# Kernel tuning notes

Measured on AMD Instinct MI355X. Metric: run time of the kernel, lower is better.

The kernel has to match this reference:

```python
import jax, jax.numpy as jnp
import numpy as np

B, L, D, Z, V, N, MAXPOS = 8, 2048, 1024, 128, 2048, 16, 2048


def setup_inputs():
    key = jax.random.key(0)
    ks = jax.random.split(key, 16)
    std = 0.02
    return {
        "x": jax.random.normal(ks[0], (B, L, D), jnp.float32),
        "norm1_w": jnp.ones((D,), jnp.float32),
        "norm1_b": jnp.zeros((D,), jnp.float32),
        "ema_delta": jax.random.normal(ks[1], (D, N), jnp.float32) * 0.2,
        "ema_alpha": jax.random.normal(ks[2], (D, N), jnp.float32) * 0.2,
        "ema_beta": jax.random.normal(ks[3], (D, N), jnp.float32) * 0.02,
        "ema_gamma": jax.random.normal(ks[4], (D, N), jnp.float32),
        "ema_omega": jax.random.normal(ks[5], (D,), jnp.float32),
        "vproj_w": jax.random.normal(ks[6], (D, V), jnp.float32) * std,
        "vproj_b": jnp.zeros((V,), jnp.float32),
        "mx_w": jax.random.normal(ks[7], (D, Z + V + 2 * D), jnp.float32) * std,
        "mx_b": jnp.zeros((Z + V + 2 * D,), jnp.float32),
        "h_w": jax.random.normal(ks[8], (V, D), jnp.float32) * std,
        "h_b": jnp.zeros((D,), jnp.float32),
        "att_gamma": jax.random.normal(ks[9], (2, Z), jnp.float32) * std,
        "att_beta": jnp.zeros((2, Z), jnp.float32),
        "rel_bias": jax.random.normal(ks[10], (2 * MAXPOS - 1,), jnp.float32) * std,
        "norm2_w": jnp.ones((D,), jnp.float32),
        "norm2_b": jnp.zeros((D,), jnp.float32),
        "ff_w1": jax.random.normal(ks[11], (D, 2 * D), jnp.float32) * std,
        "ff_b1": jnp.zeros((2 * D,), jnp.float32),
        "ff_w2": jax.random.normal(ks[12], (2 * D, D), jnp.float32) * std,
        "ff_b2": jnp.zeros((D,), jnp.float32),
    }


def _layernorm(x, w, b):
    mu = jnp.mean(x, -1, keepdims=True)
    var = jnp.mean((x - mu) ** 2, -1, keepdims=True)
    return (x - mu) * jax.lax.rsqrt(var + 1e-5) * w + b


def reference(x, norm1_w, norm1_b, ema_delta, ema_alpha, ema_beta, ema_gamma, ema_omega,
              vproj_w, vproj_b, mx_w, mx_b, h_w, h_b, att_gamma, att_beta, rel_bias,
              norm2_w, norm2_b, ff_w1, ff_b1, ff_w2, ff_b2):
    residual = x
    xn = _layernorm(x, norm1_w, norm1_b)                       # prenorm
    v = jax.nn.silu(xn @ vproj_w + vproj_b)                    # (B L V)

    # --- MultiHeadEMA (damped EMA state space) via FFT convolution ---
    p = jax.nn.sigmoid(ema_delta)                              # (D N)
    q = 1.0 - p * jax.nn.sigmoid(ema_alpha)                    # (D N) in (0,1)
    t = jnp.arange(L, dtype=jnp.float32)
    vander = jnp.exp(t[None, None, :] * jnp.log(q)[:, :, None])       # (D N L)
    kern = jnp.einsum('dnl,dn->dl', (p * ema_beta)[:, :, None] * vander,
                      ema_gamma * np.float32(1.0 / np.sqrt(N)))        # (D L)
    xT = jnp.swapaxes(xn, 1, 2)                                # (B D L)
    k_f = jnp.fft.rfft(kern, n=2 * L)
    x_f = jnp.fft.rfft(xT, n=2 * L)
    ema = jnp.fft.irfft(x_f * k_f, n=2 * L)[..., :L]           # causal conv
    mx = jax.nn.silu(jnp.swapaxes(ema, 1, 2) + xn * ema_omega) # (B L D)

    # --- moving-average gated attention ---
    base = mx @ mx_w + mx_b                                    # (B L D+Z+V+D)
    u, zr, hx = jnp.split(base, [D, D + Z + V], axis=-1)
    u = jax.nn.sigmoid(u)                                      # update gate
    zr = jax.nn.silu(zr)
    z, r = zr[..., :Z], zr[..., Z:]                            # (B L Z), (B L V)
    zqk = z[:, :, None, :] * att_gamma + att_beta              # (B L 2 Z)
    qh, kh = zqk[:, :, 0, :], zqk[:, :, 1, :]

    # simple relative positional bias: Toeplitz bias[i,j] = b[L-1 + j - i]
    bseg = rel_bias[MAXPOS - L:MAXPOS + L - 1]                 # (2L-1,)
    idx = (L - 1) + jnp.arange(L)[None, :] - jnp.arange(L)[:, None]
    bias = bseg[idx]                                           # (L L)

    qk = jnp.einsum('blz,bmz->blm', qh * np.float32(Z ** -0.5), kh) + bias
    attn = jax.nn.softmax(qk, axis=-1)                         # (B L L)
    h = jnp.einsum('blm,bmv->blv', attn, v)                    # (B L V)
    h = jax.nn.silu(hx + (h * r) @ h_w + h_b)                  # (B L D)
    out = residual + u * (h - residual)                        # addcmul gate

    # --- prenorm FFN residual block (expand=2, silu) ---
    y = _layernorm(out, norm2_w, norm2_b)
    y = jax.nn.silu(y @ ff_w1 + ff_b1) @ ff_w2 + ff_b2
    return out + y
```

## Files before the change

kernel.cpp:

```cpp
#include <hip/hip_runtime.h>
#include <hip/hip_bf16.h>
#include <cstdint>

#define B_ 8
#define L_ 2048
#define D_ 1024
#define Z_ 128
#define V_ 2048
#define N_ 16
#define NC_ 16
#define CL_ 128

typedef unsigned short ushort_t;
typedef __attribute__((ext_vector_type(8))) short short8;
typedef __attribute__((ext_vector_type(4))) float floatx4;

__device__ __forceinline__ float b2f(ushort_t u){ union{float f;unsigned i;}x; x.i=((unsigned)u)<<16; return x.f; }
__device__ __forceinline__ ushort_t f2b(float f){ union{float f;unsigned i;}x; x.f=f; unsigned r=(x.i+0x7fffu+((x.i>>16)&1u))>>16; return (ushort_t)r; }
__device__ __forceinline__ float sigmoidf_(float x){ return 1.0f/(1.0f+__expf(-x)); }
__device__ __forceinline__ float siluf_(float x){ return x/(1.0f+__expf(-x)); }

#define GLL16(g,l) __builtin_amdgcn_global_load_lds( \
    (const __attribute__((address_space(1))) void*)(g), \
    (__attribute__((address_space(3))) void*)(l), 16, 0, 0)

__device__ __forceinline__ float blockSum(float v){
  #pragma unroll
  for(int off=32;off;off>>=1) v += __shfl_xor(v,off);
  __shared__ float sm[4];
  __syncthreads();
  if((threadIdx.x&63)==0) sm[threadIdx.x>>6]=v;
  __syncthreads();
  return (sm[0]+sm[1])+(sm[2]+sm[3]);
}
__device__ __forceinline__ float blockMax(float v){
  #pragma unroll
  for(int off=32;off;off>>=1) v = fmaxf(v,__shfl_xor(v,off));
  __shared__ float sm[4];
  __syncthreads();
  if((threadIdx.x&63)==0) sm[threadIdx.x>>6]=v;
  __syncthreads();
  return fmaxf(fmaxf(sm[0],sm[1]),fmaxf(sm[2],sm[3]));
}

__global__ __launch_bounds__(256) void ln_kernel(const float* __restrict__ in,
    const float* __restrict__ w, const float* __restrict__ b,
    ushort_t* __restrict__ o16){
  const int row = blockIdx.x;
  const int t = threadIdx.x;
  const float* p = in + (size_t)row*D_;
  float4 v = *reinterpret_cast<const float4*>(p + t*4);
  float s = (v.x+v.y)+(v.z+v.w);
  s = blockSum(s);
  float mu = s*(1.0f/D_);
  float dx=v.x-mu, dy=v.y-mu, dz=v.z-mu, dw=v.w-mu;
  float ss = dx*dx+dy*dy+dz*dz+dw*dw;
  ss = blockSum(ss);
  float inv = rsqrtf(ss*(1.0f/D_)+1e-5f);
  float4 wv = *reinterpret_cast<const float4*>(w + t*4);
  float4 bv = *reinterpret_cast<const float4*>(b + t*4);
  union{ushort_t u[4]; uint2 q;} o;
  o.u[0]=f2b(dx*inv*wv.x+bv.x); o.u[1]=f2b(dy*inv*wv.y+bv.y);
  o.u[2]=f2b(dz*inv*wv.z+bv.z); o.u[3]=f2b(dw*inv*wv.w+bv.w);
  *reinterpret_cast<uint2*>(o16+(size_t)row*D_+t*4)=o.q;
}

__global__ __launch_bounds__(256) void transpose_w(const float* __restrict__ in,
    ushort_t* __restrict__ out, int R, int C){
  __shared__ float tile[32][33];
  int bx=blockIdx.x*32, by=blockIdx.y*32;
  int tx=threadIdx.x&31, ty=threadIdx.x>>5;
  #pragma unroll
  for(int i=0;i<32;i+=8) tile[ty+i][tx] = in[(size_t)(by+ty+i)*C + bx+tx];
  __syncthreads();
  #pragma unroll
  for(int i=0;i<32;i+=8) out[(size_t)(bx+ty+i)*R + by+tx] = f2b(tile[tx][ty+i]);
}

__global__ __launch_bounds__(256) void ema_setup(const float* __restrict__ delta,
    const float* __restrict__ alpha, const float* __restrict__ beta,
    const float* __restrict__ gamma, float* __restrict__ qarr,
    float* __restrict__ warr, float* __restrict__ qC){
  int i = blockIdx.x*256+threadIdx.x;
  if(i>=D_*N_) return;
  float p = sigmoidf_(delta[i]);
  float q = 1.0f - p*sigmoidf_(alpha[i]);
  qarr[i]=q; warr[i]=p*beta[i]*gamma[i]*0.25f;
  qC[i]=powf(q,(float)CL_);
}

__global__ __launch_bounds__(256) void ema_pass1(const ushort_t* __restrict__ xn,
    const float* __restrict__ qarr, float* __restrict__ E){
  int idx = blockIdx.x*256+threadIdx.x;
  int d = idx & (D_-1); int c = (idx>>10)&15; int b = idx>>14;
  const ushort_t* xp = xn + ((size_t)b*L_ + c*CL_)*D_ + d;
  float q[N_], s[N_];
  #pragma unroll
  for(int n=0;n<N_;n++){ q[n]=qarr[d*N_+n]; s[n]=0.0f; }
  for(int i=0;i<CL_;i+=8){
    float xv[8];
    #pragma unroll
    for(int j=0;j<8;j++) xv[j]=b2f(xp[(size_t)(i+j)*D_]);
    #pragma unroll
    for(int j=0;j<8;j++){
      #pragma unroll
      for(int n=0;n<N_;n++) s[n]=fmaf(q[n],s[n],xv[j]);
    }
  }
  float* Ep = E + (((size_t)b*NC_+c)*N_)*D_ + d;
  #pragma unroll
  for(int n=0;n<N_;n++) Ep[(size_t)n*D_]=s[n];
}

__global__ __launch_bounds__(256) void ema_pass2(const float* __restrict__ E,
    const float* __restrict__ qC, float* __restrict__ In){
  int idx = blockIdx.x*256+threadIdx.x;
  int d = idx & (D_-1); int b = idx>>10;
  float S[N_], qc[N_];
  #pragma unroll
  for(int n=0;n<N_;n++){ S[n]=0.0f; qc[n]=qC[d*N_+n]; }
  for(int c=0;c<NC_;c++){
    size_t base = (((size_t)b*NC_+c)*N_)*D_ + d;
    #pragma unroll
    for(int n=0;n<N_;n++) In[base+(size_t)n*D_]=S[n];
    #pragma unroll
    for(int n=0;n<N_;n++) S[n]=fmaf(qc[n],S[n],E[base+(size_t)n*D_]);
  }
}

__global__ __launch_bounds__(256) void ema_pass3_mx(const ushort_t* __restrict__ xn,
    const float* __restrict__ qarr, const float* __restrict__ warr,
    const float* __restrict__ In, const float* __restrict__ omega,
    ushort_t* __restrict__ mx){
  int idx = blockIdx.x*256+threadIdx.x;
  int d = idx & (D_-1); int c = (idx>>10)&15; int b = idx>>14;
  const ushort_t* xp = xn + ((size_t)b*L_ + c*CL_)*D_ + d;
  ushort_t* op = mx + ((size_t)b*L_ + c*CL_)*D_ + d;
  size_t base = (((size_t)b*NC_+c)*N_)*D_ + d;
  float om = omega[d];
  float q[N_], w[N_], s[N_];
  #pragma unroll
  for(int n=0;n<N_;n++){ q[n]=qarr[d*N_+n]; w[n]=warr[d*N_+n]; s[n]=In[base+(size_t)n*D_]; }
  for(int i=0;i<CL_;i+=8){
    float xv[8];
    #pragma unroll
    for(int j=0;j<8;j++) xv[j]=b2f(xp[(size_t)(i+j)*D_]);
    #pragma unroll
    for(int j=0;j<8;j++){
      float a=0.0f;
      #pragma unroll
      for(int n=0;n<N_;n++){ s[n]=fmaf(q[n],s[n],xv[j]); a=fmaf(w[n],s[n],a); }
      op[(size_t)(i+j)*D_]=f2b(siluf_(a + xv[j]*om));
    }
  }
}

__global__ __launch_bounds__(256) void softmax_kernel(const float* __restrict__ qk,
    ushort_t* __restrict__ attn){
  size_t row = blockIdx.x;
  const float* p = qk + row*(size_t)L_;
  int t = threadIdx.x;
  float vals[8];
  #pragma unroll
  for(int i=0;i<8;i++) vals[i]=p[i*256+t];
  float m=-__builtin_inff();
  #pragma unroll
  for(int i=0;i<8;i++) m=fmaxf(m,vals[i]);
  m = blockMax(m);
  float s=0.0f;
  #pragma unroll
  for(int i=0;i<8;i++){ vals[i]=__expf(vals[i]-m); s+=vals[i]; }
  s = blockSum(s);
  float inv = 1.0f/s;
  ushort_t* q = attn + row*(size_t)L_;
  #pragma unroll
  for(int i=0;i<8;i++) q[i*256+t]=f2b(vals[i]*inv);
}

#define SBAR() do{ __builtin_amdgcn_sched_barrier(0); \
    asm volatile("" ::: "memory"); \
    __builtin_amdgcn_s_barrier(); \
    asm volatile("" ::: "memory"); \
    __builtin_amdgcn_sched_barrier(0); }while(0)
#define VMW(n) asm volatile("s_waitcnt vmcnt(" #n ")" ::: "memory")

#define BAR_ACQ(vm) do{ \
    asm volatile("s_waitcnt vmcnt(" #vm ")" ::: "memory"); \
    __builtin_amdgcn_s_barrier(); \
    __builtin_amdgcn_sched_barrier(0); }while(0)
#define BAR_REL() do{ \
    __builtin_amdgcn_sched_barrier(0); \
    asm volatile("" ::: "memory"); \
    __builtin_amdgcn_s_barrier(); \
    asm volatile("" ::: "memory"); }while(0)

template<class Epi>
__global__ __launch_bounds__(256) void gemm_nt(const ushort_t* __restrict__ A,
    const ushort_t* __restrict__ B, int M, int N, int K, Epi epi){
  __shared__ __align__(16) ushort_t As[2][128*64];
  __shared__ __align__(16) ushort_t Bs[2][128*64];
  const int t = threadIdx.x;
  const int wave=t>>6, lane=t&63, quad=lane>>4, l16=lane&15;
  const int bm=blockIdx.x*128, bn=blockIdx.y*128;
  const int wm=(wave>>1)*64, wn=(wave&1)*64;
  const int srow = wave*32 + (lane>>3);
  const int schk = ((lane&7) ^ (lane>>3)) * 8;
  const ushort_t* gA[4]; const ushort_t* gB[4];
  ushort_t *lA[4], *lB[4];
  #pragma unroll
  for(int i=0;i<4;i++){
    gA[i] = A + (size_t)(bm+srow+i*8)*K + schk;
    gB[i] = B + (size_t)(bn+srow+i*8)*K + schk;
    lA[i] = &As[0][(wave*32+i*8)*64];
    lB[i] = &Bs[0][(wave*32+i*8)*64];
  }
  const ushort_t* ra[2][4]; const ushort_t* rb[2][4];
  #pragma unroll
  for(int h=0;h<2;h++)
    #pragma unroll
    for(int i=0;i<4;i++){
      int rrA = wm+i*16+l16, rrB = wn+i*16+l16;
      ra[h][i] = &As[0][rrA*64 + (((h*4+quad)^(rrA&7))*8)];
      rb[h][i] = &Bs[0][rrB*64 + (((h*4+quad)^(rrB&7))*8)];
    }
  floatx4 acc[4][4];
  #pragma unroll
  for(int i=0;i<4;i++)
    #pragma unroll
    for(int j=0;j<4;j++) acc[i][j]=(floatx4){0.f,0.f,0.f,0.f};

  const int nk = K>>6;
  #pragma unroll
  for(int i=0;i<4;i++){ GLL16(gA[i], lA[i]); GLL16(gB[i], lB[i]); }

  for(int t0=0;t0<nk;t0+=2){
    {
      const int k0=(t0+1)<<6;
      #pragma unroll
      for(int i=0;i<4;i++){ GLL16(gA[i]+k0, lA[i]+(128*64)); GLL16(gB[i]+k0, lB[i]+(128*64)); }
    }
    BAR_ACQ(8);
    #pragma unroll
    for(int h=0;h<2;h++){
      short8 af[4], bf[4];
      #pragma unroll
      for(int mt=0;mt<4;mt++) af[mt]=*reinterpret_cast<const short8*>(ra[h][mt]);
      #pragma unroll
      for(int nt=0;nt<4;nt++) bf[nt]=*reinterpret_cast<const short8*>(rb[h][nt]);
      #pragma unroll
      for(int mt=0;mt<4;mt++)
        #pragma unroll
        for(int nt=0;nt<4;nt++)
          acc[mt][nt]=__builtin_amdgcn_mfma_f32_16x16x32_bf16(af[mt],bf[nt],acc[mt][nt],0,0,0);
    }
    BAR_REL();
    if(t0+2<nk){
      const int k0=(t0+2)<<6;
      #pragma unroll
      for(int i=0;i<4;i++){ GLL16(gA[i]+k0, lA[i]); GLL16(gB[i]+k0, lB[i]); }
      BAR_ACQ(8);
    } else {
      BAR_ACQ(0);
    }
    #pragma unroll
    for(int h=0;h<2;h++){
      short8 af[4], bf[4];
      #pragma unroll
      for(int mt=0;mt<4;mt++) af[mt]=*reinterpret_cast<const short8*>(ra[h][mt]+(128*64));
      #pragma unroll
      for(int nt=0;nt<4;nt++) bf[nt]=*reinterpret_cast<const short8*>(rb[h][nt]+(128*64));
      #pragma unroll
      for(int mt=0;mt<4;mt++)
        #pragma unroll
        for(int nt=0;nt<4;nt++)
          acc[mt][nt]=__builtin_amdgcn_mfma_f32_16x16x32_bf16(af[mt],bf[nt],acc[mt][nt],0,0,0);
    }
    BAR_REL();
  }

  #pragma unroll
  for(int mt=0;mt<4;mt++)
    #pragma unroll
    for(int nt=0;nt<4;nt++)
      #pragma unroll
      for(int r=0;r<4;r++){
        int row=bm+wm+mt*16+quad*4+r;
        int col=bn+wn+nt*16+l16;
        epi(acc[mt][nt][r], row, col, 0);
      }
}


#define RDA(buf,kh,mh) \
  af[0]=pA##kh[(buf)*2048+((mh)*4+0)*128]; \
  af[1]=pA##kh[(buf)*2048+((mh)*4+1)*128]; \
  af[2]=pA##kh[(buf)*2048+((mh)*4+2)*128]; \
  af[3]=pA##kh[(buf)*2048+((mh)*4+3)*128];
#define RDB(buf,kh) \
  bf[0]=pB##kh[(buf)*2048+0*128]; \
  bf[1]=pB##kh[(buf)*2048+1*128]; \
  bf[2]=pB##kh[(buf)*2048+2*128]; \
  bf[3]=pB##kh[(buf)*2048+3*128];
#define MMA16(mh) \
  __builtin_amdgcn_s_setprio(1); \
  acc[(mh)*4+0][0]=__builtin_amdgcn_mfma_f32_16x16x32_bf16(af[0],bf[0],acc[(mh)*4+0][0],0,0,0); \
  acc[(mh)*4+0][1]=__builtin_amdgcn_mfma_f32_16x16x32_bf16(af[0],bf[1],acc[(mh)*4+0][1],0,0,0); \
  acc[(mh)*4+0][2]=__builtin_amdgcn_mfma_f32_16x16x32_bf16(af[0],bf[2],acc[(mh)*4+0][2],0,0,0); \
  acc[(mh)*4+0][3]=__builtin_amdgcn_mfma_f32_16x16x32_bf16(af[0],bf[3],acc[(mh)*4+0][3],0,0,0); \
  acc[(mh)*4+1][0]=__builtin_amdgcn_mfma_f32_16x16x32_bf16(af[1],bf[0],acc[(mh)*4+1][0],0,0,0); \
  acc[(mh)*4+1][1]=__builtin_amdgcn_mfma_f32_16x16x32_bf16(af[1],bf[1],acc[(mh)*4+1][1],0,0,0); \
  acc[(mh)*4+1][2]=__builtin_amdgcn_mfma_f32_16x16x32_bf16(af[1],bf[2],acc[(mh)*4+1][2],0,0,0); \
  acc[(mh)*4+1][3]=__builtin_amdgcn_mfma_f32_16x16x32_bf16(af[1],bf[3],acc[(mh)*4+1][3],0,0,0); \
  acc[(mh)*4+2][0]=__builtin_amdgcn_mfma_f32_16x16x32_bf16(af[2],bf[0],acc[(mh)*4+2][0],0,0,0); \
  acc[(mh)*4+2][1]=__builtin_amdgcn_mfma_f32_16x16x32_bf16(af[2],bf[1],acc[(mh)*4+2][1],0,0,0); \
  acc[(mh)*4+2][2]=__builtin_amdgcn_mfma_f32_16x16x32_bf16(af[2],bf[2],acc[(mh)*4+2][2],0,0,0); \
  acc[(mh)*4+2][3]=__builtin_amdgcn_mfma_f32_16x16x32_bf16(af[2],bf[3],acc[(mh)*4+2][3],0,0,0); \
  acc[(mh)*4+3][0]=__builtin_amdgcn_mfma_f32_16x16x32_bf16(af[3],bf[0],acc[(mh)*4+3][0],0,0,0); \
  acc[(mh)*4+3][1]=__builtin_amdgcn_mfma_f32_16x16x32_bf16(af[3],bf[1],acc[(mh)*4+3][1],0,0,0); \
  acc[(mh)*4+3][2]=__builtin_amdgcn_mfma_f32_16x16x32_bf16(af[3],bf[2],acc[(mh)*4+3][2],0,0,0); \
  acc[(mh)*4+3][3]=__builtin_amdgcn_mfma_f32_16x16x32_bf16(af[3],bf[3],acc[(mh)*4+3][3],0,0,0); \
  __builtin_amdgcn_s_setprio(0);
#define STG8(buf,k0) \
  GLL16(gA[0]+(k0), lA[0]+(buf)*16384); GLL16(gA[1]+(k0), lA[1]+(buf)*16384); \
  GLL16(gA[2]+(k0), lA[2]+(buf)*16384); GLL16(gA[3]+(k0), lA[3]+(buf)*16384); \
  GLL16(gB[0]+(k0), lB[0]+(buf)*16384); GLL16(gB[1]+(k0), lB[1]+(buf)*16384); \
  GLL16(gB[2]+(k0), lB[2]+(buf)*16384); GLL16(gB[3]+(k0), lB[3]+(buf)*16384);

#define TILE_S(buf,k0n) { \
  short8 af[4], bf[4]; \
  RDA(buf,0,0) RDB(buf,0) \
  STG8((buf)^1, k0n) \
  SBAR(); MMA16(0) SBAR(); \
  RDA(buf,0,1) \
  SBAR(); MMA16(1) SBAR(); \
  RDA(buf,1,0) RDB(buf,1) \
  SBAR(); MMA16(0) SBAR(); \
  RDA(buf,1,1) \
  SBAR(); MMA16(1) VMW(0); SBAR(); \
}
#define TILE_L(buf) { \
  short8 af[4], bf[4]; \
  RDA(buf,0,0) RDB(buf,0) \
  SBAR(); MMA16(0) SBAR(); \
  RDA(buf,0,1) \
  SBAR(); MMA16(1) SBAR(); \
  RDA(buf,1,0) RDB(buf,1) \
  SBAR(); MMA16(0) SBAR(); \
  RDA(buf,1,1) \
  SBAR(); MMA16(1) \
}

template<class Epi>
__global__ __launch_bounds__(512) void gemm_nt2(const ushort_t* __restrict__ A0,
    const ushort_t* __restrict__ B0, int M, int N, int K,
    size_t za, size_t zb, Epi epi){
  __shared__ __align__(16) ushort_t As[2*256*64];
  __shared__ __align__(16) ushort_t Bs[2*256*64];
  const int t = threadIdx.x;
  const int wave=t>>6, lane=t&63, quad=lane>>4, l16=lane&15;
  int bx, by;
  {
    int gx=gridDim.x, gy=gridDim.y;
    int f = blockIdx.y*gx + blockIdx.x;
    if((gy==4 || gy==8) && (gx%(32/gy))==0){
      int GW = 32/gy, nst = gx/GW;
      int s, r;
      if((nst&7)==0){ int xc=f&7; int j=f>>3; s = xc*(nst>>3) + (j>>5); r = j&31; }
      else { s = f>>5; r = f&31; }
      bx = s*GW + (r%GW); by = r/GW;
    } else { bx = blockIdx.x; by = blockIdx.y; }
  }
  const int z = blockIdx.z;
  const ushort_t* A = A0 + (size_t)z*za;
  const ushort_t* B = B0 + (size_t)z*zb;
  const int bm=bx*256, bn=by*256;
  const int wm=(wave>>2)*128, wn=(wave&3)*64;
  const int roff = lane>>3;
  const int goff = ((lane&7)^(lane>>3))*8;
  const ushort_t* gA[4]; const ushort_t* gB[4];
  ushort_t* lA[4]; ushort_t* lB[4];
  #pragma unroll
  for(int i=0;i<4;i++){
    gA[i] = A + (size_t)(bm + wave*32 + i*8 + roff)*K + goff;
    gB[i] = B + (size_t)(bn + wave*32 + i*8 + roff)*K + goff;
    lA[i] = As + (wave*32 + i*8)*64;
    lB[i] = Bs + (wave*32 + i*8)*64;
  }
  const short8* pA0 = reinterpret_cast<const short8*>(As) + (wm+l16)*8 + ((quad  )^(l16&7));
  const short8* pA1 = reinterpret_cast<const short8*>(As) + (wm+l16)*8 + ((quad^4)^(l16&7));
  const short8* pB0 = reinterpret_cast<const short8*>(Bs) + (wn+l16)*8 + ((quad  )^(l16&7));
  const short8* pB1 = reinterpret_cast<const short8*>(Bs) + (wn+l16)*8 + ((quad^4)^(l16&7));
  floatx4 acc[8][4];
  #pragma unroll
  for(int i=0;i<8;i++)
    #pragma unroll
    for(int j=0;j<4;j++) acc[i][j]=(floatx4){0.f,0.f,0.f,0.f};

  const int nkt = K>>6;
  STG8(0, 0)
  VMW(0); SBAR();

  for(int t0=0; t0+2<nkt; t0+=2){
    TILE_S(0,(t0+1)<<6)
    TILE_S(1,(t0+2)<<6)
  }
  TILE_S(0,(nkt-1)<<6)
  TILE_L(1)

  #pragma unroll
  for(int mt=0;mt<8;mt++)
    #pragma unroll
    for(int nt=0;nt<4;nt++)
      #pragma unroll
      for(int r=0;r<4;r++){
        int row=bm+wm+mt*16+quad*4+r;
        int col=bn+wn+nt*16+l16;
        epi(acc[mt][nt][r], row, col, z);
      }
}

struct EpiV {
  ushort_t* vT; const float* vb;
  __device__ void operator()(float v,int row,int col,int) const {
    float s = siluf_(v + vb[col]);
    int b = row>>11, l = row&(L_-1);
    vT[((size_t)b*V_ + col)*L_ + l] = f2b(s);
  }
};
struct EpiU {
  ushort_t* u; const float* mxb;
  __device__ void operator()(float v,int row,int col,int) const {
    u[(size_t)row*D_+col]=f2b(sigmoidf_(v+mxb[col]));
  }
};
struct EpiQKh {
  ushort_t* qh; ushort_t* kh; const float* mxb; const float* ag; const float* ab;
  __device__ void operator()(float v,int row,int col,int) const {
    float z=siluf_(v+mxb[col]);
    qh[(size_t)row*Z_+col]=f2b(z*ag[col]+ab[col]);
    kh[(size_t)row*Z_+col]=f2b(z*ag[Z_+col]+ab[Z_+col]);
  }
};
struct EpiR {
  ushort_t* r; const float* mxb;
  __device__ void operator()(float v,int row,int col,int) const {
    r[(size_t)row*V_+col]=f2b(siluf_(v+mxb[col]));
  }
};
struct EpiHx {
  ushort_t* hx; const float* mxb;
  __device__ void operator()(float v,int row,int col,int) const {
    hx[(size_t)row*D_+col]=f2b(v+mxb[col]);
  }
};
struct EpiQK {
  float* qk; const float* rb;
  __device__ void operator()(float v,int row,int col,int) const {
    qk[(size_t)row*L_+col] = v*0.08838834764831845f + rb[L_-1+col-row];
  }
};
struct EpiH {
  ushort_t* hr; const ushort_t* r;
  __device__ void operator()(float v,int row,int col,int z) const {
    size_t idx = ((size_t)z*L_ + row)*V_ + col;
    hr[idx] = f2b(v * b2f(r[idx]));
  }
};
struct EpiOut {
  float* out; const float* x; const ushort_t* u; const ushort_t* hx; const float* hb;
  __device__ void operator()(float v,int row,int col,int) const {
    size_t idx=(size_t)row*D_+col;
    float h2 = siluf_(b2f(hx[idx]) + v + hb[col]);
    float xv = x[idx];
    out[idx] = xv + b2f(u[idx])*(h2-xv);
  }
};
struct EpiF1 {
  ushort_t* f1; const float* b1;
  __device__ void operator()(float v,int row,int col,int) const {
    f1[(size_t)row*(2*D_)+col]=f2b(siluf_(v+b1[col]));
  }
};
struct EpiFinal {
  float* dout; const float* b2;
  __device__ void operator()(float v,int row,int col,int) const {
    size_t idx=(size_t)row*D_+col;
    dout[idx] = dout[idx] + v + b2[col];
  }
};

extern "C" void kernel_launch(void* const* d_in, const int* in_sizes, int n_in,
                              void* d_out, int out_size, void* d_ws, size_t ws_size,
                              hipStream_t stream){
  const float* x        = (const float*)d_in[0];
  const float* norm1_w  = (const float*)d_in[1];
  const float* norm1_b  = (const float*)d_in[2];
  const float* ema_delta= (const float*)d_in[3];
  const float* ema_alpha= (const float*)d_in[4];
  const float* ema_beta = (const float*)d_in[5];
  const float* ema_gamma= (const float*)d_in[6];
  const float* ema_omega= (const float*)d_in[7];
  const float* vproj_w  = (const float*)d_in[8];
  const float* vproj_b  = (const float*)d_in[9];
  const float* mx_w     = (const float*)d_in[10];
  const float* mx_b     = (const float*)d_in[11];
  const float* h_w      = (const float*)d_in[12];
  const float* h_b      = (const float*)d_in[13];
  const float* att_gamma= (const float*)d_in[14];
  const float* att_beta = (const float*)d_in[15];
  const float* rel_bias = (const float*)d_in[16];
  const float* norm2_w  = (const float*)d_in[17];
  const float* norm2_b  = (const float*)d_in[18];
  const float* ff_w1    = (const float*)d_in[19];
  const float* ff_b1    = (const float*)d_in[20];
  const float* ff_w2    = (const float*)d_in[21];
  const float* ff_b2    = (const float*)d_in[22];
  float* dout = (float*)d_out;
  char* ws = (char*)d_ws;

  size_t cur = 0;
  auto take = [&](size_t b)->size_t{ size_t o=cur; cur += (b+255)&~255ull; return o; };
  const size_t o_wvT  = take((size_t)V_*D_*2);
  const size_t o_wmxT = take((size_t)4224*D_*2);
  const size_t o_whT  = take((size_t)D_*V_*2);
  const size_t o_wf1T = take((size_t)2*D_*D_*2);
  const size_t o_wf2T = take((size_t)D_*2*D_*2);
  const size_t o_qarr = take((size_t)D_*N_*4);
  const size_t o_warr = take((size_t)D_*N_*4);
  const size_t o_qC   = take((size_t)D_*N_*4);
  const size_t globals_end = cur;

  int g = 0;
  size_t o_xn=0,o_mx=0,o_u=0,o_hx=0,o_r=0,o_qh=0,o_kh=0,o_qk=0,o_at=0;
  for(int cand=8; cand>=1; cand>>=1){
    cur = globals_end;
    size_t xn_o = take((size_t)cand*L_*D_*2);
    size_t mx_o = take((size_t)cand*L_*D_*2);
    size_t u_o  = take((size_t)cand*L_*D_*2);
    size_t hx_o = take((size_t)cand*L_*D_*2);
    size_t r_o  = take((size_t)cand*L_*V_*2);
    size_t qh_o = take((size_t)cand*L_*Z_*2);
    size_t kh_o = take((size_t)cand*L_*Z_*2);
    size_t qk_o, at_o;
    if(cand>=4){ qk_o = xn_o; at_o = xn_o + (size_t)L_*L_*4; }
    else { qk_o = take((size_t)L_*L_*4); at_o = take((size_t)L_*L_*2); }
    if(cur <= ws_size){
      g=cand; o_xn=xn_o; o_mx=mx_o; o_u=u_o; o_hx=hx_o; o_r=r_o;
      o_qh=qh_o; o_kh=kh_o; o_qk=qk_o; o_at=at_o; break;
    }
  }
  if(!g) return;

  ushort_t* wvT  = (ushort_t*)(ws+o_wvT);
  ushort_t* wmxT = (ushort_t*)(ws+o_wmxT);
  ushort_t* whT  = (ushort_t*)(ws+o_whT);
  ushort_t* wf1T = (ushort_t*)(ws+o_wf1T);
  ushort_t* wf2T = (ushort_t*)(ws+o_wf2T);
  float* qarr = (float*)(ws+o_qarr);
  float* warr = (float*)(ws+o_warr);
  float* qC   = (float*)(ws+o_qC);
  ushort_t* xn  = (ushort_t*)(ws+o_xn);
  ushort_t* mx  = (ushort_t*)(ws+o_mx);
  ushort_t* u16 = (ushort_t*)(ws+o_u);
  ushort_t* hx16= (ushort_t*)(ws+o_hx);
  ushort_t* r16 = (ushort_t*)(ws+o_r);
  ushort_t* qh  = (ushort_t*)(ws+o_qh);
  ushort_t* kh  = (ushort_t*)(ws+o_kh);
  float*    qk  = (float*)   (ws+o_qk);
  ushort_t* attn= (ushort_t*)(ws+o_at);
  float*    E   = (float*)(ws+o_u);
  float*    In  = (float*)(ws+o_hx);
  ushort_t* ybf = xn;
  ushort_t* f1  = r16;

  int nbat; ushort_t* attnB;
  if(g>=4){ nbat = g/2; attnB = mx; }
  else    { nbat = 1;   attnB = attn; }

  transpose_w<<<dim3(V_/32, D_/32), 256, 0, stream>>>(vproj_w, wvT, D_, V_);
  transpose_w<<<dim3(4224/32, D_/32), 256, 0, stream>>>(mx_w, wmxT, D_, 4224);
  transpose_w<<<dim3(D_/32, V_/32), 256, 0, stream>>>(h_w, whT, V_, D_);
  transpose_w<<<dim3((2*D_)/32, D_/32), 256, 0, stream>>>(ff_w1, wf1T, D_, 2*D_);
  transpose_w<<<dim3(D_/32, (2*D_)/32), 256, 0, stream>>>(ff_w2, wf2T, 2*D_, D_);
  ema_setup<<<(D_*N_)/256, 256, 0, stream>>>(ema_delta, ema_alpha, ema_beta, ema_gamma, qarr, warr, qC);

  for(int gi=0; gi<B_/g; ++gi){
    const int RG = g*L_;
    const float* x_g  = x    + (size_t)gi*RG*D_;
    float*       do_g = dout + (size_t)gi*RG*D_;
    ushort_t*    vT   = (ushort_t*)do_g;

    ln_kernel<<<RG, 256, 0, stream>>>(x_g, norm1_w, norm1_b, xn);
    ema_pass1<<<(g*NC_*D_)/256, 256, 0, stream>>>(xn, qarr, E);
    ema_pass2<<<(g*D_)/256, 256, 0, stream>>>(E, qC, In);
    ema_pass3_mx<<<(g*NC_*D_)/256, 256, 0, stream>>>(xn, qarr, warr, In, ema_omega, mx);

    { EpiV e{vT, vproj_b};
      gemm_nt2<<<dim3(RG/256, V_/256), 512, 0, stream>>>(xn, wvT, RG, V_, D_, 0, 0, e); }

    { EpiU e{u16, mx_b};
      gemm_nt2<<<dim3(RG/256, D_/256), 512, 0, stream>>>(mx, wmxT, RG, D_, D_, 0, 0, e); }
    { EpiQKh e{qh, kh, mx_b+D_, att_gamma, att_beta};
      gemm_nt<<<dim3(RG/128, Z_/128), 256, 0, stream>>>(mx, wmxT+(size_t)D_*D_, RG, Z_, D_, e); }
    { EpiR e{r16, mx_b+D_+Z_};
      gemm_nt2<<<dim3(RG/256, V_/256), 512, 0, stream>>>(mx, wmxT+(size_t)(D_+Z_)*D_, RG, V_, D_, 0, 0, e); }
    { EpiHx e{hx16, mx_b+D_+Z_+V_};
      gemm_nt2<<<dim3(RG/256, D_/256), 512, 0, stream>>>(mx, wmxT+(size_t)(D_+Z_+V_)*D_, RG, D_, D_, 0, 0, e); }

    for(int q0=0; q0<g; q0+=nbat){
      for(int bi=q0; bi<q0+nbat; ++bi){
        { EpiQK e{qk, rel_bias};
          gemm_nt<<<dim3(L_/128, L_/128), 256, 0, stream>>>(
            qh+(size_t)bi*L_*Z_, kh+(size_t)bi*L_*Z_, L_, L_, Z_, e); }
        softmax_kernel<<<L_, 256, 0, stream>>>(qk, attnB+(size_t)(bi-q0)*L_*L_);
      }
      { EpiH e{r16+(size_t)q0*L_*V_, r16+(size_t)q0*L_*V_};
        gemm_nt2<<<dim3(L_/256, V_/256, nbat), 512, 0, stream>>>(
          attnB, vT+(size_t)q0*V_*L_, L_, V_, L_,
          (size_t)L_*L_, (size_t)V_*L_, e); }
    }

    { EpiOut e{do_g, x_g, u16, hx16, h_b};
      gemm_nt2<<<dim3(RG/256, D_/256), 512, 0, stream>>>(r16, whT, RG, D_, V_, 0, 0, e); }
    ln_kernel<<<RG, 256, 0, stream>>>(do_g, norm2_w, norm2_b, ybf);
    { EpiF1 e{f1, ff_b1};
      gemm_nt2<<<dim3(RG/256, (2*D_)/256), 512, 0, stream>>>(ybf, wf1T, RG, 2*D_, D_, 0, 0, e); }
    { EpiFinal e{do_g, ff_b2};
      gemm_nt2<<<dim3(RG/256, D_/256), 512, 0, stream>>>(f1, wf2T, RG, D_, 2*D_, 0, 0, e); }
  }
}
```

Before: 1.354 ms.

## Split GEMM LDS tiles into k-halves and stagger async loads across phases

Reorganizes the 256x256 bf16 GEMM's shared-memory staging into two 32-wide k-halves, each with its own swizzle. Global-to-LDS loads for the next tile are now spread across the four MMA phases, with partial vmcnt waits instead of one full wait per tile. This aims to overlap memory traffic with MFMA work and shorten stalls at tile boundaries. It also drops the sched_barrier fences around the barriers, which gives the compiler more scheduling freedom but risks reordering LDS accesses across synchronisation points.

```diff
diff --git a/kernel.cpp b/kernel.cpp
--- a/kernel.cpp
+++ b/kernel.cpp
@@ -177,19 +177,13 @@
   for(int i=0;i<8;i++) q[i*256+t]=f2b(vals[i]*inv);
 }
 
-#define SBAR() do{ __builtin_amdgcn_sched_barrier(0); \
-    asm volatile("" ::: "memory"); \
-    __builtin_amdgcn_s_barrier(); \
-    asm volatile("" ::: "memory"); \
-    __builtin_amdgcn_sched_barrier(0); }while(0)
+#define BAR() __builtin_amdgcn_s_barrier()
 #define VMW(n) asm volatile("s_waitcnt vmcnt(" #n ")" ::: "memory")
 
 #define BAR_ACQ(vm) do{ \
     asm volatile("s_waitcnt vmcnt(" #vm ")" ::: "memory"); \
-    __builtin_amdgcn_s_barrier(); \
-    __builtin_amdgcn_sched_barrier(0); }while(0)
+    __builtin_amdgcn_s_barrier(); }while(0)
 #define BAR_REL() do{ \
-    __builtin_amdgcn_sched_barrier(0); \
     asm volatile("" ::: "memory"); \
     __builtin_amdgcn_s_barrier(); \
     asm volatile("" ::: "memory"); }while(0)
@@ -291,16 +285,16 @@
 }
 
 
-#define RDA(buf,kh,mh) \
-  af[0]=pA##kh[(buf)*2048+((mh)*4+0)*128]; \
-  af[1]=pA##kh[(buf)*2048+((mh)*4+1)*128]; \
-  af[2]=pA##kh[(buf)*2048+((mh)*4+2)*128]; \
-  af[3]=pA##kh[(buf)*2048+((mh)*4+3)*128];
-#define RDB(buf,kh) \
-  bf[0]=pB##kh[(buf)*2048+0*128]; \
-  bf[1]=pB##kh[(buf)*2048+1*128]; \
-  bf[2]=pB##kh[(buf)*2048+2*128]; \
-  bf[3]=pB##kh[(buf)*2048+3*128];
+#define RA4(buf,kh,mh) \
+  af[0]=pA8[(buf)*2048+(kh)*1024+((mh)*4+0)*64+rowA]; \
+  af[1]=pA8[(buf)*2048+(kh)*1024+((mh)*4+1)*64+rowA]; \
+  af[2]=pA8[(buf)*2048+(kh)*1024+((mh)*4+2)*64+rowA]; \
+  af[3]=pA8[(buf)*2048+(kh)*1024+((mh)*4+3)*64+rowA];
+#define RB4(buf,kh) \
+  bf[0]=pB8[(buf)*2048+(kh)*1024+0*64+rowB]; \
+  bf[1]=pB8[(buf)*2048+(kh)*1024+1*64+rowB]; \
+  bf[2]=pB8[(buf)*2048+(kh)*1024+2*64+rowB]; \
+  bf[3]=pB8[(buf)*2048+(kh)*1024+3*64+rowB];
 #define MMA16(mh) \
   __builtin_amdgcn_s_setprio(1); \
   acc[(mh)*4+0][0]=__builtin_amdgcn_mfma_f32_16x16x32_bf16(af[0],bf[0],acc[(mh)*4+0][0],0,0,0); \
@@ -320,42 +314,46 @@
   acc[(mh)*4+3][2]=__builtin_amdgcn_mfma_f32_16x16x32_bf16(af[3],bf[2],acc[(mh)*4+3][2],0,0,0); \
   acc[(mh)*4+3][3]=__builtin_amdgcn_mfma_f32_16x16x32_bf16(af[3],bf[3],acc[(mh)*4+3][3],0,0,0); \
   __builtin_amdgcn_s_setprio(0);
-#define STG8(buf,k0) \
-  GLL16(gA[0]+(k0), lA[0]+(buf)*16384); GLL16(gA[1]+(k0), lA[1]+(buf)*16384); \
-  GLL16(gA[2]+(k0), lA[2]+(buf)*16384); GLL16(gA[3]+(k0), lA[3]+(buf)*16384); \
-  GLL16(gB[0]+(k0), lB[0]+(buf)*16384); GLL16(gB[1]+(k0), lB[1]+(buf)*16384); \
-  GLL16(gB[2]+(k0), lB[2]+(buf)*16384); GLL16(gB[3]+(k0), lB[3]+(buf)*16384);
-
-#define TILE_S(buf,k0n) { \
+#define SA2(b,kh,k0) \
+  GLL16(gA0+(k0)+(kh)*32, lAd+((b)*2+(kh))*8192); \
+  GLL16(gA1+(k0)+(kh)*32, lAd+((b)*2+(kh))*8192+512);
+#define SB2(b,kh,k0) \
+  GLL16(gB0+(k0)+(kh)*32, lBd+((b)*2+(kh))*8192); \
+  GLL16(gB1+(k0)+(kh)*32, lBd+((b)*2+(kh))*8192+512);
+
+#define TILE_S(buf,k1) { \
   short8 af[4], bf[4]; \
-  RDA(buf,0,0) RDB(buf,0) \
-  STG8((buf)^1, k0n) \
-  SBAR(); MMA16(0) SBAR(); \
-  RDA(buf,0,1) \
-  SBAR(); MMA16(1) SBAR(); \
-  RDA(buf,1,0) RDB(buf,1) \
-  SBAR(); MMA16(0) SBAR(); \
-  RDA(buf,1,1) \
-  SBAR(); MMA16(1) VMW(0); SBAR(); \
-}
-#define TILE_L(buf) { \
+  RA4(buf,0,0) RB4(buf,0) \
+  SA2((buf)^1,0,k1) \
+  BAR(); MMA16(0) BAR(); \
+  RA4(buf,0,1) \
+  SB2((buf)^1,0,k1) \
+  BAR(); MMA16(1) VMW(4); BAR(); \
+  RA4(buf,1,0) RB4(buf,1) \
+  SA2((buf)^1,1,k1) \
+  BAR(); MMA16(0) BAR(); \
+  RA4(buf,1,1) \
+  SB2((buf)^1,1,k1) \
+  BAR(); MMA16(1) VMW(4); BAR(); \
+}
+#define TILE_E(buf) { \
   short8 af[4], bf[4]; \
-  RDA(buf,0,0) RDB(buf,0) \
-  SBAR(); MMA16(0) SBAR(); \
-  RDA(buf,0,1) \
-  SBAR(); MMA16(1) SBAR(); \
-  RDA(buf,1,0) RDB(buf,1) \
-  SBAR(); MMA16(0) SBAR(); \
-  RDA(buf,1,1) \
-  SBAR(); MMA16(1) \
+  RA4(buf,0,0) RB4(buf,0) \
+  BAR(); MMA16(0) BAR(); \
+  RA4(buf,0,1) \
+  BAR(); MMA16(1) VMW(0); BAR(); \
+  RA4(buf,1,0) RB4(buf,1) \
+  BAR(); MMA16(0) BAR(); \
+  RA4(buf,1,1) \
+  BAR(); MMA16(1) \
 }
 
 template<class Epi>
 __global__ __launch_bounds__(512) void gemm_nt2(const ushort_t* __restrict__ A0,
     const ushort_t* __restrict__ B0, int M, int N, int K,
     size_t za, size_t zb, Epi epi){
-  __shared__ __align__(16) ushort_t As[2*256*64];
-  __shared__ __align__(16) ushort_t Bs[2*256*64];
+  __shared__ __align__(16) ushort_t As[2*2*8192];
+  __shared__ __align__(16) ushort_t Bs[2*2*8192];
   const int t = threadIdx.x;
   const int wave=t>>6, lane=t&63, quad=lane>>4, l16=lane&15;
   int bx, by;
@@ -375,21 +373,18 @@
   const ushort_t* B = B0 + (size_t)z*zb;
   const int bm=bx*256, bn=by*256;
   const int wm=(wave>>2)*128, wn=(wave&3)*64;
-  const int roff = lane>>3;
-  const int goff = ((lane&7)^(lane>>3))*8;
-  const ushort_t* gA[4]; const ushort_t* gB[4];
-  ushort_t* lA[4]; ushort_t* lB[4];
-  #pragma unroll
-  for(int i=0;i<4;i++){
-    gA[i] = A + (size_t)(bm + wave*32 + i*8 + roff)*K + goff;
-    gB[i] = B + (size_t)(bn + wave*32 + i*8 + roff)*K + goff;
-    lA[i] = As + (wave*32 + i*8)*64;
-    lB[i] = Bs + (wave*32 + i*8)*64;
-  }
-  const short8* pA0 = reinterpret_cast<const short8*>(As) + (wm+l16)*8 + ((quad  )^(l16&7));
-  const short8* pA1 = reinterpret_cast<const short8*>(As) + (wm+l16)*8 + ((quad^4)^(l16&7));
-  const short8* pB0 = reinterpret_cast<const short8*>(Bs) + (wn+l16)*8 + ((quad  )^(l16&7));
-  const short8* pB1 = reinterpret_cast<const short8*>(Bs) + (wn+l16)*8 + ((quad^4)^(l16&7));
+  const int g8 = ((lane&3) ^ ((lane>>3)&3))*8;
+  const ushort_t* gA0 = A + (size_t)(bm + wave*32 + (lane>>2))*K + g8;
+  const ushort_t* gA1 = gA0 + (size_t)16*K;
+  const ushort_t* gB0 = B + (size_t)(bn + wave*32 + (lane>>2))*K + g8;
+  const ushort_t* gB1 = gB0 + (size_t)16*K;
+  ushort_t* lAd = As + wave*1024;
+  ushort_t* lBd = Bs + wave*1024;
+  const short8* pA8 = reinterpret_cast<const short8*>(As);
+  const short8* pB8 = reinterpret_cast<const short8*>(Bs);
+  const int swl = (l16>>1)&3;
+  const int rowA = (wm+l16)*4 + (quad^swl);
+  const int rowB = (wn+l16)*4 + (quad^swl);
   floatx4 acc[8][4];
   #pragma unroll
   for(int i=0;i<8;i++)
@@ -397,15 +392,15 @@
     for(int j=0;j<4;j++) acc[i][j]=(floatx4){0.f,0.f,0.f,0.f};
 
   const int nkt = K>>6;
-  STG8(0, 0)
-  VMW(0); SBAR();
+  SA2(0,0,0) SB2(0,0,0) SA2(0,1,0) SB2(0,1,0)
+  VMW(4); BAR();
 
   for(int t0=0; t0+2<nkt; t0+=2){
     TILE_S(0,(t0+1)<<6)
     TILE_S(1,(t0+2)<<6)
   }
   TILE_S(0,(nkt-1)<<6)
-  TILE_L(1)
+  TILE_E(1)
 
   #pragma unroll
   for(int mt=0;mt<8;mt++)
```

After: 1.267 ms. -6.5%, faster.
